# Performance work log

Measured on AMD Instinct MI355X. Metric: run time of the kernel, lower is better.

The kernel has to match this reference:

```python
import jax, jax.numpy as jnp
import numpy as np
from jax import lax

LN_EPS = 1e-5

def _conv1d(h, w, b):
    # h: [N, L, Cin], w: [Cout, Cin, K] (torch Conv1d layout), padding=1
    out = lax.conv_general_dilated(h, w, window_strides=(1,), padding=[(1, 1)],
                                   dimension_numbers=("NWC", "OIW", "NWC"))
    return out + b

def _layer_norm(h, g, b):
    m = jnp.mean(h, axis=-1, keepdims=True)
    v = jnp.mean((h - m) ** 2, axis=-1, keepdims=True)
    return (h - m) * lax.rsqrt(v + LN_EPS) * g + b

def setup_inputs() -> dict:
    key = jax.random.key(0)
    ks = jax.random.split(key, 8)
    N, L, D, F = 32, 512, 384, 256
    return {
        "x": jax.random.normal(ks[0], (N, L, D), jnp.float32),
        "conv1_w": jax.random.normal(ks[1], (F, D, 3), jnp.float32) * 0.05,
        "conv1_b": jnp.zeros((F,), jnp.float32),
        "ln1_g": jnp.ones((F,), jnp.float32),
        "ln1_b": jnp.zeros((F,), jnp.float32),
        "conv2_w": jax.random.normal(ks[2], (F, F, 3), jnp.float32) * 0.05,
        "conv2_b": jnp.zeros((F,), jnp.float32),
        "ln2_g": jnp.ones((F,), jnp.float32),
        "ln2_b": jnp.zeros((F,), jnp.float32),
        "lin_w": jax.random.normal(ks[3], (F,), jnp.float32) * 0.05,
        "lin_b": jnp.zeros((), jnp.float32),
        "target": jax.random.randint(ks[4], (N, L), 0, 8, dtype=jnp.int32),
        "mel_max_length": 2048,
    }

def reference(x, conv1_w, conv1_b, ln1_g, ln1_b, conv2_w, conv2_b, ln2_g, ln2_b,
              lin_w, lin_b, target, mel_max_length):
    # Duration predictor (dropout is identity at inference)
    h = jax.nn.relu(_layer_norm(_conv1d(x, conv1_w, conv1_b), ln1_g, ln1_b))
    h = jax.nn.relu(_layer_norm(_conv1d(h, conv2_w, conv2_b), ln2_g, ln2_b))
    duration_predictor_output = jnp.einsum("nlf,f->nl", h, lin_w) + lin_b  # [N, L]

    # LR: frame t copies phoneme j iff cumsum(dur)[:j] <= t < cumsum(dur)[:j+1]
    # (equivalent to the one-hot alignment matmul, padded to mel_max_length)
    N, L, D = x.shape
    T = mel_max_length
    cums = jnp.cumsum(target, axis=-1)                      # [N, L]
    frames = jnp.arange(T, dtype=cums.dtype)                # [T]
    idx = jax.vmap(lambda c: jnp.searchsorted(c, frames, side="right"))(cums)  # [N, T]
    valid = frames[None, :] < cums[:, -1:]                  # frames beyond total are zero
    gathered = jnp.take_along_axis(x, jnp.clip(idx, 0, L - 1)[:, :, None], axis=1)
    output = gathered * valid[:, :, None].astype(x.dtype)   # [N, T, D]
    return output, duration_predictor_output
```

## Files before the change

### kernel.cpp

```cpp
#include <hip/hip_runtime.h>
#include <hip/hip_bf16.h>

typedef unsigned short u16;
typedef short s8v __attribute__((ext_vector_type(8)));
typedef float f4v __attribute__((ext_vector_type(4)));
typedef u16 u16x8 __attribute__((ext_vector_type(8)));

static __device__ __forceinline__ u16 f2bf(float v) {
    __hip_bfloat16 h = __float2bfloat16(v);
    return *(u16*)&h;
}

__global__ __launch_bounds__(256) void gather_prep_kernel(
    const float* __restrict__ x,
    const int*   __restrict__ target,
    const float* __restrict__ w1,
    const float* __restrict__ w2,
    u16* __restrict__ Wt1,
    u16* __restrict__ Wt2,
    float* __restrict__ out0)
{
    __shared__ int c[512];
    __shared__ int ridx[64];
    const int b = blockIdx.x, tid = threadIdx.x;

    if (b >= 1024) {
        if (b < 2176) {
            const int K = 1152, DIN = 384;
            int e = (b - 1024) * 256 + tid;
            int f = e / K;
            int rem = e - f * K;
            int kc = rem / DIN;
            int d = rem - kc * DIN;
            Wt1[e] = f2bf(w1[f * K + d * 3 + kc]);
        } else {
            const int K = 768, DIN = 256;
            int e = (b - 2176) * 256 + tid;
            int f = e / K;
            int rem = e - f * K;
            int kc = rem / DIN;
            int d = rem - kc * DIN;
            Wt2[e] = f2bf(w2[f * K + d * 3 + kc]);
        }
        return;
    }

    const int n = b >> 5, sub = b & 31;
    c[tid]       = target[n * 512 + tid];
    c[tid + 256] = target[n * 512 + 256 + tid];
    __syncthreads();
    for (int off = 1; off < 512; off <<= 1) {
        int v0 = (tid       >= off) ? c[tid       - off] : 0;
        int v1 = (tid + 256 >= off) ? c[tid + 256 - off] : 0;
        __syncthreads();
        c[tid]       += v0;
        c[tid + 256] += v1;
        __syncthreads();
    }
    const int total = c[511];
    if (tid < 64) {
        int t = sub * 64 + tid;
        int lo = 0, hi = 512;
        while (lo < hi) {
            int mid = (lo + hi) >> 1;
            if (c[mid] <= t) lo = mid + 1; else hi = mid;
        }
        ridx[tid] = (t < total) ? min(lo, 511) : -1;
    }
    __syncthreads();

    const size_t xbase = (size_t)(n << 9) * 384;
    const size_t obase = ((size_t)(n << 11) + sub * 64) * 384;
    #pragma unroll 4
    for (int it = 0; it < 12; ++it) {
        int u  = tid + it * 256;
        int j  = u % 48;
        int rl = u / 48;
        int ie = ridx[rl];
        f4v v0 = {0.f, 0.f, 0.f, 0.f}, v1 = v0;
        if (ie >= 0) {
            const float* src = &x[xbase + (size_t)ie * 384];
            v0 = *(const f4v*)&src[j * 4];
            v1 = *(const f4v*)&src[(j + 48) * 4];
        }
        float* dst = &out0[obase + (size_t)rl * 384];
        __builtin_nontemporal_store(v0, (f4v*)&dst[j * 4]);
        __builtin_nontemporal_store(v1, (f4v*)&dst[(j + 48) * 4]);
    }
}

__global__ __launch_bounds__(256, 2) void fused_conv_kernel(
    const float* __restrict__ x,
    const u16* __restrict__ Wt1,
    const u16* __restrict__ Wt2,
    const float* __restrict__ cb1, const float* __restrict__ g1,
    const float* __restrict__ bb1,
    const float* __restrict__ cb2, const float* __restrict__ g2,
    const float* __restrict__ bb2,
    const float* __restrict__ lw, const float* __restrict__ lbp,
    float* __restrict__ dpo)
{
    __shared__ __align__(128) char LDS[73216];
    char* Bs    = LDS + 38400;
    float* redS = (float*)(LDS + 71168);
    float* redQ = (float*)(LDS + 71936);
    float* redP = (float*)(LDS + 72704);

    const int tid  = threadIdx.x;
    const int lane = tid & 63, wc = tid >> 6;
    const int lr = lane & 15, q4 = lane >> 4;
    const int sb = (blockIdx.x & 7) * 64 + (blockIdx.x >> 3);
    const int m0 = sb * 32;
    const int n  = m0 >> 9, l0 = m0 & 511;

    const int b_r    = tid >> 3;
    const int b_slot = (tid & 7) ^ (b_r & 7);
    int boff[4];
    #pragma unroll
    for (int ni = 0; ni < 4; ni++) boff[ni] = (64 * wc + 16 * ni + lr) * 128;
    const int slot0 = ((q4)     ^ (lr & 7)) << 4;
    const int slot1 = ((q4 | 4) ^ (lr & 7)) << 4;

    for (int u = tid; u < 2400; u += 256) {
        int j = u / 48, s = u - j * 48;
        int lp = l0 - 9 + j;
        f4v v0 = {0.f, 0.f, 0.f, 0.f}, v1 = v0;
        if (lp >= 0 && lp < 512) {
            const float* src = x + ((size_t)((n << 9) + lp)) * 384 + s * 8;
            v0 = *(const f4v*)src;
            v1 = *(const f4v*)(src + 4);
        }
        u16x8 r;
        #pragma unroll
        for (int jj = 0; jj < 4; jj++) { r[jj] = f2bf(v0[jj]); r[4 + jj] = f2bf(v1[jj]); }
        int ss = (s & ~7) | ((s & 7) ^ (j & 7));
        *(u16x8*)(LDS + j * 768 + ss * 16) = r;
    }

    auto xwread = [&](int j, int s) -> s8v {
        int ss = (s & ~7) | ((s & 7) ^ (j & 7));
        return *(const s8v*)(LDS + j * 768 + (ss << 4));
    };

    f4v acc[3][4];
    #pragma unroll
    for (int mi = 0; mi < 3; mi++)
        #pragma unroll
        for (int ni = 0; ni < 4; ni++) acc[mi][ni] = {0.f, 0.f, 0.f, 0.f};

    for (int t = 0; t < 18; ++t) {
        __syncthreads();
        const int k0 = t * 64;
        const u16* bsrc = Wt1 + (size_t)b_r * 1152 + k0 + b_slot * 8;
        #pragma unroll
        for (int q = 0; q < 8; q++) {
            __builtin_amdgcn_global_load_lds(
                (const __attribute__((address_space(1))) void*)(bsrc + (size_t)q * 32 * 1152),
                (__attribute__((address_space(3))) void*)(Bs + q * 4096 + tid * 16),
                16, 0, 0);
        }
        __syncthreads();

        const int kc = k0 / 384;
        const int s0 = (k0 - kc * 384) >> 3;
        #pragma unroll
        for (int kk = 0; kk < 2; kk++) {
            const int sl = kk ? slot1 : slot0;
            const int s  = s0 + 4 * kk + q4;
            s8v a0 = xwread(lr + kc,      s);
            s8v a1 = xwread(16 + lr + kc, s);
            s8v a2 = xwread(32 + lr + kc, s);
            s8v b0 = *(const s8v*)(Bs + boff[0] + sl);
            s8v b1 = *(const s8v*)(Bs + boff[1] + sl);
            s8v b2 = *(const s8v*)(Bs + boff[2] + sl);
            s8v b3 = *(const s8v*)(Bs + boff[3] + sl);
            acc[0][0] = __builtin_amdgcn_mfma_f32_16x16x32_bf16(a0, b0, acc[0][0], 0, 0, 0);
            acc[0][1] = __builtin_amdgcn_mfma_f32_16x16x32_bf16(a0, b1, acc[0][1], 0, 0, 0);
            acc[0][2] = __builtin_amdgcn_mfma_f32_16x16x32_bf16(a0, b2, acc[0][2], 0, 0, 0);
            acc[0][3] = __builtin_amdgcn_mfma_f32_16x16x32_bf16(a0, b3, acc[0][3], 0, 0, 0);
            acc[1][0] = __builtin_amdgcn_mfma_f32_16x16x32_bf16(a1, b0, acc[1][0], 0, 0, 0);
            acc[1][1] = __builtin_amdgcn_mfma_f32_16x16x32_bf16(a1, b1, acc[1][1], 0, 0, 0);
            acc[1][2] = __builtin_amdgcn_mfma_f32_16x16x32_bf16(a1, b2, acc[1][2], 0, 0, 0);
            acc[1][3] = __builtin_amdgcn_mfma_f32_16x16x32_bf16(a1, b3, acc[1][3], 0, 0, 0);
            acc[2][0] = __builtin_amdgcn_mfma_f32_16x16x32_bf16(a2, b0, acc[2][0], 0, 0, 0);
            acc[2][1] = __builtin_amdgcn_mfma_f32_16x16x32_bf16(a2, b1, acc[2][1], 0, 0, 0);
            acc[2][2] = __builtin_amdgcn_mfma_f32_16x16x32_bf16(a2, b2, acc[2][2], 0, 0, 0);
            acc[2][3] = __builtin_amdgcn_mfma_f32_16x16x32_bf16(a2, b3, acc[2][3], 0, 0, 0);
        }
    }

    int col[4];
    float cbv[4], gv[4], bbv[4];
    #pragma unroll
    for (int ni = 0; ni < 4; ni++) {
        col[ni] = 64 * wc + 16 * ni + lr;
        cbv[ni] = cb1[col[ni]]; gv[ni] = g1[col[ni]]; bbv[ni] = bb1[col[ni]];
    }

    #pragma unroll
    for (int mi = 0; mi < 3; mi++)
        #pragma unroll
        for (int reg = 0; reg < 4; reg++) {
            float s = 0.f, q = 0.f;
            #pragma unroll
            for (int ni = 0; ni < 4; ni++) {
                float v = acc[mi][ni][reg] + cbv[ni];
                s += v; q += v * v;
            }
            #pragma unroll
            for (int msk = 1; msk < 16; msk <<= 1) {
                s += __shfl_xor(s, msk);
                q += __shfl_xor(q, msk);
            }
            if (lr == 0) {
                int rl = 16 * mi + 4 * q4 + reg;
                redS[rl * 4 + wc] = s;
                redQ[rl * 4 + wc] = q;
            }
        }
    __syncthreads();

    #pragma unroll
    for (int mi = 0; mi < 3; mi++)
        #pragma unroll
        for (int reg = 0; reg < 4; reg++) {
            int rl = 16 * mi + 4 * q4 + reg;
            int h  = rl - 7;
            if (h >= 0 && h < 34) {
                float4 ps = *(float4*)&redS[rl * 4];
                float4 pq = *(float4*)&redQ[rl * 4];
                float mean = (ps.x + ps.y + ps.z + ps.w) * (1.f / 256.f);
                float var  = (pq.x + pq.y + pq.z + pq.w) * (1.f / 256.f) - mean * mean;
                float rs   = rsqrtf(var + 1e-5f);
                int l = l0 - 8 + rl;
                bool lv = (l >= 0 && l < 512);
                #pragma unroll
                for (int ni = 0; ni < 4; ni++) {
                    float v = acc[mi][ni][reg] + cbv[ni];
                    float o = lv ? fmaxf(0.f, (v - mean) * rs * gv[ni] + bbv[ni]) : 0.f;
                    int slot = (col[ni] >> 3) ^ (h & 7);
                    *(u16*)(LDS + h * 512 + slot * 16 + (col[ni] & 7) * 2) = f2bf(o);
                }
            }
        }

    f4v acc2[2][4];
    #pragma unroll
    for (int mi = 0; mi < 2; mi++)
        #pragma unroll
        for (int ni = 0; ni < 4; ni++) acc2[mi][ni] = {0.f, 0.f, 0.f, 0.f};

    for (int t2 = 0; t2 < 12; ++t2) {
        __syncthreads();
        const int k0 = t2 * 64;
        const u16* bsrc = Wt2 + (size_t)b_r * 768 + k0 + b_slot * 8;
        #pragma unroll
        for (int q = 0; q < 8; q++) {
            __builtin_amdgcn_global_load_lds(
                (const __attribute__((address_space(1))) void*)(bsrc + (size_t)q * 32 * 768),
                (__attribute__((address_space(3))) void*)(Bs + q * 4096 + tid * 16),
                16, 0, 0);
        }
        __syncthreads();

        const int kc2   = t2 >> 2;
        const int sbase = 8 * (t2 & 3);
        #pragma unroll
        for (int kk = 0; kk < 2; kk++) {
            const int sl = kk ? slot1 : slot0;
            s8v b0 = *(const s8v*)(Bs + boff[0] + sl);
            s8v b1 = *(const s8v*)(Bs + boff[1] + sl);
            s8v b2 = *(const s8v*)(Bs + boff[2] + sl);
            s8v b3 = *(const s8v*)(Bs + boff[3] + sl);
            s8v a0, a1;
            {
                int h = lr + kc2;
                int s = sbase + 4 * kk + q4;
                a0 = *(const s8v*)(LDS + h * 512 + ((s ^ (h & 7)) << 4));
                h = 16 + lr + kc2;
                a1 = *(const s8v*)(LDS + h * 512 + ((s ^ (h & 7)) << 4));
            }
            acc2[0][0] = __builtin_amdgcn_mfma_f32_16x16x32_bf16(a0, b0, acc2[0][0], 0, 0, 0);
            acc2[0][1] = __builtin_amdgcn_mfma_f32_16x16x32_bf16(a0, b1, acc2[0][1], 0, 0, 0);
            acc2[0][2] = __builtin_amdgcn_mfma_f32_16x16x32_bf16(a0, b2, acc2[0][2], 0, 0, 0);
            acc2[0][3] = __builtin_amdgcn_mfma_f32_16x16x32_bf16(a0, b3, acc2[0][3], 0, 0, 0);
            acc2[1][0] = __builtin_amdgcn_mfma_f32_16x16x32_bf16(a1, b0, acc2[1][0], 0, 0, 0);
            acc2[1][1] = __builtin_amdgcn_mfma_f32_16x16x32_bf16(a1, b1, acc2[1][1], 0, 0, 0);
            acc2[1][2] = __builtin_amdgcn_mfma_f32_16x16x32_bf16(a1, b2, acc2[1][2], 0, 0, 0);
            acc2[1][3] = __builtin_amdgcn_mfma_f32_16x16x32_bf16(a1, b3, acc2[1][3], 0, 0, 0);
        }
    }

    float cbv2[4], gv2[4], bbv2[4], lwv[4];
    #pragma unroll
    for (int ni = 0; ni < 4; ni++) {
        cbv2[ni] = cb2[col[ni]]; gv2[ni] = g2[col[ni]]; bbv2[ni] = bb2[col[ni]];
        lwv[ni]  = lw[col[ni]];
    }

    float sv[2][4], sq[2][4];
    #pragma unroll
    for (int mi = 0; mi < 2; mi++)
        #pragma unroll
        for (int reg = 0; reg < 4; reg++) {
            float s = 0.f, q = 0.f;
            #pragma unroll
            for (int ni = 0; ni < 4; ni++) {
                float v = acc2[mi][ni][reg] + cbv2[ni];
                s += v; q += v * v;
            }
            #pragma unroll
            for (int msk = 1; msk < 16; msk <<= 1) {
                s += __shfl_xor(s, msk);
                q += __shfl_xor(q, msk);
            }
            sv[mi][reg] = s; sq[mi][reg] = q;
        }
    __syncthreads();
    if (lr == 0) {
        #pragma unroll
        for (int mi = 0; mi < 2; mi++)
            #pragma unroll
            for (int reg = 0; reg < 4; reg++) {
                int rl = 16 * mi + 4 * q4 + reg;
                redS[rl * 4 + wc] = sv[mi][reg];
                redQ[rl * 4 + wc] = sq[mi][reg];
            }
    }
    __syncthreads();

    float pp[2][4];
    #pragma unroll
    for (int mi = 0; mi < 2; mi++)
        #pragma unroll
        for (int reg = 0; reg < 4; reg++) {
            int rl = 16 * mi + 4 * q4 + reg;
            float4 ps = *(float4*)&redS[rl * 4];
            float4 pq = *(float4*)&redQ[rl * 4];
            float mean = (ps.x + ps.y + ps.z + ps.w) * (1.f / 256.f);
            float var  = (pq.x + pq.y + pq.z + pq.w) * (1.f / 256.f) - mean * mean;
            float rs   = rsqrtf(var + 1e-5f);
            float p = 0.f;
            #pragma unroll
            for (int ni = 0; ni < 4; ni++) {
                float v = acc2[mi][ni][reg] + cbv2[ni];
                float o = fmaxf(0.f, (v - mean) * rs * gv2[ni] + bbv2[ni]);
                p += o * lwv[ni];
            }
            #pragma unroll
            for (int msk = 1; msk < 16; msk <<= 1) p += __shfl_xor(p, msk);
            pp[mi][reg] = p;
        }
    if (lr == 0) {
        #pragma unroll
        for (int mi = 0; mi < 2; mi++)
            #pragma unroll
            for (int reg = 0; reg < 4; reg++) {
                int rl = 16 * mi + 4 * q4 + reg;
                redP[rl * 4 + wc] = pp[mi][reg];
            }
    }
    __syncthreads();
    if (tid < 32) {
        float4 p4 = *(float4*)&redP[tid * 4];
        dpo[m0 + tid] = p4.x + p4.y + p4.z + p4.w + lbp[0];
    }
}

extern "C" void kernel_launch(void* const* d_in, const int* in_sizes, int n_in,
                              void* d_out, int out_size, void* d_ws, size_t ws_size,
                              hipStream_t stream) {
    const float* x   = (const float*)d_in[0];
    const float* w1  = (const float*)d_in[1];
    const float* b1  = (const float*)d_in[2];
    const float* g1  = (const float*)d_in[3];
    const float* bb1 = (const float*)d_in[4];
    const float* w2  = (const float*)d_in[5];
    const float* b2  = (const float*)d_in[6];
    const float* g2  = (const float*)d_in[7];
    const float* bb2 = (const float*)d_in[8];
    const float* lw  = (const float*)d_in[9];
    const float* lb  = (const float*)d_in[10];
    const int* target = (const int*)d_in[11];

    char* wsb = (char*)d_ws;
    u16*  Wt1 = (u16*)wsb;
    u16*  Wt2 = (u16*)(wsb + 589824);

    float* out0 = (float*)d_out;
    float* dpo  = out0 + (size_t)32 * 2048 * 384;

    gather_prep_kernel<<<2944, 256, 0, stream>>>(
        x, target, w1, w2, Wt1, Wt2, out0);

    fused_conv_kernel<<<512, 256, 0, stream>>>(
        x, Wt1, Wt2, b1, g1, bb1, b2, g2, bb2, lw, lb, dpo);
}
```

Measured before the change: 67.65 us.

## Double-buffer weight tiles with half-size K steps in both conv GEMM loops

Replaces the single 32KB weight tile (K=64 per step, two syncs per step) with two 16KB buffers holding K=32 each. The next tile's global-to-LDS load is issued before computing on the current one, so weight fetch latency overlaps the MFMA work and each step needs only one barrier. The LDS swizzle is changed to fit the 64-byte row layout. In exchange there are twice as many iterations and barriers per step, and each step has less MFMA work to hide the load behind. The code also appears to rely on the barrier at the end of each iteration to cover the async LDS load's completion, with no explicit wait on it.

```diff
diff --git a/kernel.cpp b/kernel.cpp
--- a/kernel.cpp
+++ b/kernel.cpp
@@ -101,7 +101,7 @@
     float* __restrict__ dpo)
 {
     __shared__ __align__(128) char LDS[73216];
-    char* Bs    = LDS + 38400;
+    char* Bs0   = LDS + 38400;
     float* redS = (float*)(LDS + 71168);
     float* redQ = (float*)(LDS + 71936);
     float* redP = (float*)(LDS + 72704);
@@ -113,13 +113,12 @@
     const int m0 = sb * 32;
     const int n  = m0 >> 9, l0 = m0 & 511;
 
-    const int b_r    = tid >> 3;
-    const int b_slot = (tid & 7) ^ (b_r & 7);
+    const int b_r32   = tid >> 2;
+    const int b_slot32 = (tid & 3) ^ ((tid >> 3) & 3);
     int boff[4];
     #pragma unroll
-    for (int ni = 0; ni < 4; ni++) boff[ni] = (64 * wc + 16 * ni + lr) * 128;
-    const int slot0 = ((q4)     ^ (lr & 7)) << 4;
-    const int slot1 = ((q4 | 4) ^ (lr & 7)) << 4;
+    for (int ni = 0; ni < 4; ni++) boff[ni] = (64 * wc + 16 * ni + lr) * 64;
+    const int bslot = (q4 ^ ((lr >> 1) & 3)) << 4;
 
     for (int u = tid; u < 2400; u += 256) {
         int j = u / 48, s = u - j * 48;
@@ -142,38 +141,41 @@
         return *(const s8v*)(LDS + j * 768 + (ss << 4));
     };
 
-    f4v acc[3][4];
-    #pragma unroll
-    for (int mi = 0; mi < 3; mi++)
-        #pragma unroll
-        for (int ni = 0; ni < 4; ni++) acc[mi][ni] = {0.f, 0.f, 0.f, 0.f};
-
-    for (int t = 0; t < 18; ++t) {
-        __syncthreads();
-        const int k0 = t * 64;
-        const u16* bsrc = Wt1 + (size_t)b_r * 1152 + k0 + b_slot * 8;
-        #pragma unroll
-        for (int q = 0; q < 8; q++) {
+    auto stageB = [&](const u16* __restrict__ Wt, int K, int buf, int t) {
+        const int k0 = t * 32;
+        const u16* bsrc = Wt + (size_t)b_r32 * K + k0 + b_slot32 * 8;
+        char* Bs = Bs0 + buf * 16384;
+        #pragma unroll
+        for (int q = 0; q < 4; q++) {
             __builtin_amdgcn_global_load_lds(
-                (const __attribute__((address_space(1))) void*)(bsrc + (size_t)q * 32 * 1152),
+                (const __attribute__((address_space(1))) void*)(bsrc + (size_t)q * 64 * K),
                 (__attribute__((address_space(3))) void*)(Bs + q * 4096 + tid * 16),
                 16, 0, 0);
         }
-        __syncthreads();
-
-        const int kc = k0 / 384;
-        const int s0 = (k0 - kc * 384) >> 3;
-        #pragma unroll
-        for (int kk = 0; kk < 2; kk++) {
-            const int sl = kk ? slot1 : slot0;
-            const int s  = s0 + 4 * kk + q4;
+    };
+
+    f4v acc[3][4];
+    #pragma unroll
+    for (int mi = 0; mi < 3; mi++)
+        #pragma unroll
+        for (int ni = 0; ni < 4; ni++) acc[mi][ni] = {0.f, 0.f, 0.f, 0.f};
+
+    stageB(Wt1, 1152, 0, 0);
+    __syncthreads();
+    int cur = 0;
+    for (int t = 0; t < 36; ++t) {
+        if (t + 1 < 36) stageB(Wt1, 1152, cur ^ 1, t + 1);
+        {
+            char* Bs = Bs0 + cur * 16384;
+            const int kc = t / 12;
+            const int s  = (t % 12) * 4 + q4;
             s8v a0 = xwread(lr + kc,      s);
             s8v a1 = xwread(16 + lr + kc, s);
             s8v a2 = xwread(32 + lr + kc, s);
-            s8v b0 = *(const s8v*)(Bs + boff[0] + sl);
-            s8v b1 = *(const s8v*)(Bs + boff[1] + sl);
-            s8v b2 = *(const s8v*)(Bs + boff[2] + sl);
-            s8v b3 = *(const s8v*)(Bs + boff[3] + sl);
+            s8v b0 = *(const s8v*)(Bs + boff[0] + bslot);
+            s8v b1 = *(const s8v*)(Bs + boff[1] + bslot);
+            s8v b2 = *(const s8v*)(Bs + boff[2] + bslot);
+            s8v b3 = *(const s8v*)(Bs + boff[3] + bslot);
             acc[0][0] = __builtin_amdgcn_mfma_f32_16x16x32_bf16(a0, b0, acc[0][0], 0, 0, 0);
             acc[0][1] = __builtin_amdgcn_mfma_f32_16x16x32_bf16(a0, b1, acc[0][1], 0, 0, 0);
             acc[0][2] = __builtin_amdgcn_mfma_f32_16x16x32_bf16(a0, b2, acc[0][2], 0, 0, 0);
@@ -187,6 +189,8 @@
             acc[2][2] = __builtin_amdgcn_mfma_f32_16x16x32_bf16(a2, b2, acc[2][2], 0, 0, 0);
             acc[2][3] = __builtin_amdgcn_mfma_f32_16x16x32_bf16(a2, b3, acc[2][3], 0, 0, 0);
         }
+        __syncthreads();
+        cur ^= 1;
     }
 
     int col[4];
@@ -250,32 +254,22 @@
         #pragma unroll
         for (int ni = 0; ni < 4; ni++) acc2[mi][ni] = {0.f, 0.f, 0.f, 0.f};
 
-    for (int t2 = 0; t2 < 12; ++t2) {
-        __syncthreads();
-        const int k0 = t2 * 64;
-        const u16* bsrc = Wt2 + (size_t)b_r * 768 + k0 + b_slot * 8;
-        #pragma unroll
-        for (int q = 0; q < 8; q++) {
-            __builtin_amdgcn_global_load_lds(
-                (const __attribute__((address_space(1))) void*)(bsrc + (size_t)q * 32 * 768),
-                (__attribute__((address_space(3))) void*)(Bs + q * 4096 + tid * 16),
-                16, 0, 0);
-        }
-        __syncthreads();
-
-        const int kc2   = t2 >> 2;
-        const int sbase = 8 * (t2 & 3);
-        #pragma unroll
-        for (int kk = 0; kk < 2; kk++) {
-            const int sl = kk ? slot1 : slot0;
-            s8v b0 = *(const s8v*)(Bs + boff[0] + sl);
-            s8v b1 = *(const s8v*)(Bs + boff[1] + sl);
-            s8v b2 = *(const s8v*)(Bs + boff[2] + sl);
-            s8v b3 = *(const s8v*)(Bs + boff[3] + sl);
+    stageB(Wt2, 768, 0, 0);
+    __syncthreads();
+    cur = 0;
+    for (int t2 = 0; t2 < 24; ++t2) {
+        if (t2 + 1 < 24) stageB(Wt2, 768, cur ^ 1, t2 + 1);
+        {
+            char* Bs = Bs0 + cur * 16384;
+            const int kc2 = t2 >> 3;
+            const int s   = (t2 & 7) * 4 + q4;
+            s8v b0 = *(const s8v*)(Bs + boff[0] + bslot);
+            s8v b1 = *(const s8v*)(Bs + boff[1] + bslot);
+            s8v b2 = *(const s8v*)(Bs + boff[2] + bslot);
+            s8v b3 = *(const s8v*)(Bs + boff[3] + bslot);
             s8v a0, a1;
             {
                 int h = lr + kc2;
-                int s = sbase + 4 * kk + q4;
                 a0 = *(const s8v*)(LDS + h * 512 + ((s ^ (h & 7)) << 4));
                 h = 16 + lr + kc2;
                 a1 = *(const s8v*)(LDS + h * 512 + ((s ^ (h & 7)) << 4));
@@ -289,6 +283,8 @@
             acc2[1][2] = __builtin_amdgcn_mfma_f32_16x16x32_bf16(a1, b2, acc2[1][2], 0, 0, 0);
             acc2[1][3] = __builtin_amdgcn_mfma_f32_16x16x32_bf16(a1, b3, acc2[1][3], 0, 0, 0);
         }
+        __syncthreads();
+        cur ^= 1;
     }
 
     float cbv2[4], gv2[4], bbv2[4], lwv[4];
```

Result: slower. 74.41 us (+10.0%).

## Register-prefetch weight tiles and shrink input halo staging in fused conv kernel

Applied to the files above, without the earlier changes.

Replaces the synchronous global_load_lds weight staging with register prefetch of the next K-tile. The loads are issued before the current tile's MFMAs and written to LDS afterwards, so global latency overlaps compute. The x staging buffer is cut from 50 to 36 rows by storing only the 34 rows with real data and clamping reads of the halo rows. Those halo rows only feed conv1 rows that are zeroed or never used. The smaller LDS footprint may allow higher occupancy, at the cost of extra VGPRs for the prefetch registers and a clamp on every A read.

```diff
diff --git a/kernel.cpp b/kernel.cpp
--- a/kernel.cpp
+++ b/kernel.cpp
@@ -100,11 +100,11 @@
     const float* __restrict__ lw, const float* __restrict__ lbp,
     float* __restrict__ dpo)
 {
-    __shared__ __align__(128) char LDS[73216];
-    char* Bs    = LDS + 38400;
-    float* redS = (float*)(LDS + 71168);
-    float* redQ = (float*)(LDS + 71936);
-    float* redP = (float*)(LDS + 72704);
+    __shared__ __align__(128) char LDS[62464];
+    char* Bs    = LDS + 27648;
+    float* redS = (float*)(LDS + 60416);
+    float* redQ = (float*)(LDS + 61184);
+    float* redP = (float*)(LDS + 61952);
 
     const int tid  = threadIdx.x;
     const int lane = tid & 63, wc = tid >> 6;
@@ -121,9 +121,22 @@
     const int slot0 = ((q4)     ^ (lr & 7)) << 4;
     const int slot1 = ((q4 | 4) ^ (lr & 7)) << 4;
 
-    for (int u = tid; u < 2400; u += 256) {
-        int j = u / 48, s = u - j * 48;
-        int lp = l0 - 9 + j;
+    auto loadB = [&](const u16* __restrict__ Wt, int K, int t, s8v* bv) {
+        const int k0 = t * 64;
+        const u16* bsrc = Wt + (size_t)b_r * K + k0 + b_slot * 8;
+        #pragma unroll
+        for (int q = 0; q < 8; q++)
+            bv[q] = *(const s8v*)(bsrc + (size_t)q * 32 * K);
+    };
+    auto writeB = [&](const s8v* bv) {
+        #pragma unroll
+        for (int q = 0; q < 8; q++)
+            *(s8v*)(Bs + q * 4096 + tid * 16) = bv[q];
+    };
+
+    for (int u = tid; u < 1728; u += 256) {
+        int j7 = u / 48, s = u - j7 * 48;
+        int lp = l0 - 2 + j7;
         f4v v0 = {0.f, 0.f, 0.f, 0.f}, v1 = v0;
         if (lp >= 0 && lp < 512) {
             const float* src = x + ((size_t)((n << 9) + lp)) * 384 + s * 8;
@@ -133,13 +146,14 @@
         u16x8 r;
         #pragma unroll
         for (int jj = 0; jj < 4; jj++) { r[jj] = f2bf(v0[jj]); r[4 + jj] = f2bf(v1[jj]); }
-        int ss = (s & ~7) | ((s & 7) ^ (j & 7));
-        *(u16x8*)(LDS + j * 768 + ss * 16) = r;
+        int ss = (s & ~7) | ((s & 7) ^ (j7 & 7));
+        *(u16x8*)(LDS + j7 * 768 + ss * 16) = r;
     }
 
     auto xwread = [&](int j, int s) -> s8v {
-        int ss = (s & ~7) | ((s & 7) ^ (j & 7));
-        return *(const s8v*)(LDS + j * 768 + (ss << 4));
+        int j7 = min(max(j, 7), 42) - 7;
+        int ss = (s & ~7) | ((s & 7) ^ (j7 & 7));
+        return *(const s8v*)(LDS + j7 * 768 + (ss << 4));
     };
 
     f4v acc[3][4];
@@ -148,44 +162,50 @@
         #pragma unroll
         for (int ni = 0; ni < 4; ni++) acc[mi][ni] = {0.f, 0.f, 0.f, 0.f};
 
+    {
+        s8v bv[8];
+        loadB(Wt1, 1152, 0, bv);
+        writeB(bv);
+    }
+    __syncthreads();
+
     for (int t = 0; t < 18; ++t) {
+        s8v nv[8];
+        const bool pre = (t + 1 < 18);
+        if (pre) loadB(Wt1, 1152, t + 1, nv);
+        {
+            const int k0 = t * 64;
+            const int kc = k0 / 384;
+            const int s0 = (k0 - kc * 384) >> 3;
+            #pragma unroll
+            for (int kk = 0; kk < 2; kk++) {
+                const int sl = kk ? slot1 : slot0;
+                const int s  = s0 + 4 * kk + q4;
+                s8v a0 = xwread(lr + kc,      s);
+                s8v a1 = xwread(16 + lr + kc, s);
+                s8v a2 = xwread(32 + lr + kc, s);
+                s8v b0 = *(const s8v*)(Bs + boff[0] + sl);
+                s8v b1 = *(const s8v*)(Bs + boff[1] + sl);
+                s8v b2 = *(const s8v*)(Bs + boff[2] + sl);
+                s8v b3 = *(const s8v*)(Bs + boff[3] + sl);
+                acc[0][0] = __builtin_amdgcn_mfma_f32_16x16x32_bf16(a0, b0, acc[0][0], 0, 0, 0);
+                acc[0][1] = __builtin_amdgcn_mfma_f32_16x16x32_bf16(a0, b1, acc[0][1], 0, 0, 0);
+                acc[0][2] = __builtin_amdgcn_mfma_f32_16x16x32_bf16(a0, b2, acc[0][2], 0, 0, 0);
+                acc[0][3] = __builtin_amdgcn_mfma_f32_16x16x32_bf16(a0, b3, acc[0][3], 0, 0, 0);
+                acc[1][0] = __builtin_amdgcn_mfma_f32_16x16x32_bf16(a1, b0, acc[1][0], 0, 0, 0);
+                acc[1][1] = __builtin_amdgcn_mfma_f32_16x16x32_bf16(a1, b1, acc[1][1], 0, 0, 0);
+                acc[1][2] = __builtin_amdgcn_mfma_f32_16x16x32_bf16(a1, b2, acc[1][2], 0, 0, 0);
+                acc[1][3] = __builtin_amdgcn_mfma_f32_16x16x32_bf16(a1, b3, acc[1][3], 0, 0, 0);
+                acc[2][0] = __builtin_amdgcn_mfma_f32_16x16x32_bf16(a2, b0, acc[2][0], 0, 0, 0);
+                acc[2][1] = __builtin_amdgcn_mfma_f32_16x16x32_bf16(a2, b1, acc[2][1], 0, 0, 0);
+                acc[2][2] = __builtin_amdgcn_mfma_f32_16x16x32_bf16(a2, b2, acc[2][2], 0, 0, 0);
+                acc[2][3] = __builtin_amdgcn_mfma_f32_16x16x32_bf16(a2, b3, acc[2][3], 0, 0, 0);
+            }
+        }
         __syncthreads();
-        const int k0 = t * 64;
-        const u16* bsrc = Wt1 + (size_t)b_r * 1152 + k0 + b_slot * 8;
-        #pragma unroll
-        for (int q = 0; q < 8; q++) {
-            __builtin_amdgcn_global_load_lds(
-                (const __attribute__((address_space(1))) void*)(bsrc + (size_t)q * 32 * 1152),
-                (__attribute__((address_space(3))) void*)(Bs + q * 4096 + tid * 16),
-                16, 0, 0);
-        }
-        __syncthreads();
-
-        const int kc = k0 / 384;
-        const int s0 = (k0 - kc * 384) >> 3;
-        #pragma unroll
-        for (int kk = 0; kk < 2; kk++) {
-            const int sl = kk ? slot1 : slot0;
-            const int s  = s0 + 4 * kk + q4;
-            s8v a0 = xwread(lr + kc,      s);
-            s8v a1 = xwread(16 + lr + kc, s);
-            s8v a2 = xwread(32 + lr + kc, s);
-            s8v b0 = *(const s8v*)(Bs + boff[0] + sl);
-            s8v b1 = *(const s8v*)(Bs + boff[1] + sl);
-            s8v b2 = *(const s8v*)(Bs + boff[2] + sl);
-            s8v b3 = *(const s8v*)(Bs + boff[3] + sl);
-            acc[0][0] = __builtin_amdgcn_mfma_f32_16x16x32_bf16(a0, b0, acc[0][0], 0, 0, 0);
-            acc[0][1] = __builtin_amdgcn_mfma_f32_16x16x32_bf16(a0, b1, acc[0][1], 0, 0, 0);
-            acc[0][2] = __builtin_amdgcn_mfma_f32_16x16x32_bf16(a0, b2, acc[0][2], 0, 0, 0);
-            acc[0][3] = __builtin_amdgcn_mfma_f32_16x16x32_bf16(a0, b3, acc[0][3], 0, 0, 0);
-            acc[1][0] = __builtin_amdgcn_mfma_f32_16x16x32_bf16(a1, b0, acc[1][0], 0, 0, 0);
-            acc[1][1] = __builtin_amdgcn_mfma_f32_16x16x32_bf16(a1, b1, acc[1][1], 0, 0, 0);
-            acc[1][2] = __builtin_amdgcn_mfma_f32_16x16x32_bf16(a1, b2, acc[1][2], 0, 0, 0);
-            acc[1][3] = __builtin_amdgcn_mfma_f32_16x16x32_bf16(a1, b3, acc[1][3], 0, 0, 0);
-            acc[2][0] = __builtin_amdgcn_mfma_f32_16x16x32_bf16(a2, b0, acc[2][0], 0, 0, 0);
-            acc[2][1] = __builtin_amdgcn_mfma_f32_16x16x32_bf16(a2, b1, acc[2][1], 0, 0, 0);
-            acc[2][2] = __builtin_amdgcn_mfma_f32_16x16x32_bf16(a2, b2, acc[2][2], 0, 0, 0);
-            acc[2][3] = __builtin_amdgcn_mfma_f32_16x16x32_bf16(a2, b3, acc[2][3], 0, 0, 0);
+        if (pre) {
+            writeB(nv);
+            __syncthreads();
         }
     }
 
@@ -250,44 +270,49 @@
         #pragma unroll
         for (int ni = 0; ni < 4; ni++) acc2[mi][ni] = {0.f, 0.f, 0.f, 0.f};
 
+    {
+        s8v bv[8];
+        loadB(Wt2, 768, 0, bv);
+        writeB(bv);
+    }
+    __syncthreads();
+
     for (int t2 = 0; t2 < 12; ++t2) {
+        s8v nv[8];
+        const bool pre = (t2 + 1 < 12);
+        if (pre) loadB(Wt2, 768, t2 + 1, nv);
+        {
+            const int kc2   = t2 >> 2;
+            const int sbase = 8 * (t2 & 3);
+            #pragma unroll
+            for (int kk = 0; kk < 2; kk++) {
+                const int sl = kk ? slot1 : slot0;
+                s8v b0 = *(const s8v*)(Bs + boff[0] + sl);
+                s8v b1 = *(const s8v*)(Bs + boff[1] + sl);
+                s8v b2 = *(const s8v*)(Bs + boff[2] + sl);
+                s8v b3 = *(const s8v*)(Bs + boff[3] + sl);
+                s8v a0, a1;
+                {
+                    int h = lr + kc2;
+                    int s = sbase + 4 * kk + q4;
+                    a0 = *(const s8v*)(LDS + h * 512 + ((s ^ (h & 7)) << 4));
+                    h = 16 + lr + kc2;
+                    a1 = *(const s8v*)(LDS + h * 512 + ((s ^ (h & 7)) << 4));
+                }
+                acc2[0][0] = __builtin_amdgcn_mfma_f32_16x16x32_bf16(a0, b0, acc2[0][0], 0, 0, 0);
+                acc2[0][1] = __builtin_amdgcn_mfma_f32_16x16x32_bf16(a0, b1, acc2[0][1], 0, 0, 0);
+                acc2[0][2] = __builtin_amdgcn_mfma_f32_16x16x32_bf16(a0, b2, acc2[0][2], 0, 0, 0);
+                acc2[0][3] = __builtin_amdgcn_mfma_f32_16x16x32_bf16(a0, b3, acc2[0][3], 0, 0, 0);
+                acc2[1][0] = __builtin_amdgcn_mfma_f32_16x16x32_bf16(a1, b0, acc2[1][0], 0, 0, 0);
+                acc2[1][1] = __builtin_amdgcn_mfma_f32_16x16x32_bf16(a1, b1, acc2[1][1], 0, 0, 0);
+                acc2[1][2] = __builtin_amdgcn_mfma_f32_16x16x32_bf16(a1, b2, acc2[1][2], 0, 0, 0);
+                acc2[1][3] = __builtin_amdgcn_mfma_f32_16x16x32_bf16(a1, b3, acc2[1][3], 0, 0, 0);
+            }
+        }
         __syncthreads();
-        const int k0 = t2 * 64;
-        const u16* bsrc = Wt2 + (size_t)b_r * 768 + k0 + b_slot * 8;
-        #pragma unroll
-        for (int q = 0; q < 8; q++) {
-            __builtin_amdgcn_global_load_lds(
-                (const __attribute__((address_space(1))) void*)(bsrc + (size_t)q * 32 * 768),
-                (__attribute__((address_space(3))) void*)(Bs + q * 4096 + tid * 16),
-                16, 0, 0);
-        }
-        __syncthreads();
-
-        const int kc2   = t2 >> 2;
-        const int sbase = 8 * (t2 & 3);
-        #pragma unroll
-        for (int kk = 0; kk < 2; kk++) {
-            const int sl = kk ? slot1 : slot0;
-            s8v b0 = *(const s8v*)(Bs + boff[0] + sl);
-            s8v b1 = *(const s8v*)(Bs + boff[1] + sl);
-            s8v b2 = *(const s8v*)(Bs + boff[2] + sl);
-            s8v b3 = *(const s8v*)(Bs + boff[3] + sl);
-            s8v a0, a1;
-            {
-                int h = lr + kc2;
-                int s = sbase + 4 * kk + q4;
-                a0 = *(const s8v*)(LDS + h * 512 + ((s ^ (h & 7)) << 4));
-                h = 16 + lr + kc2;
-                a1 = *(const s8v*)(LDS + h * 512 + ((s ^ (h & 7)) << 4));
-            }
-            acc2[0][0] = __builtin_amdgcn_mfma_f32_16x16x32_bf16(a0, b0, acc2[0][0], 0, 0, 0);
-            acc2[0][1] = __builtin_amdgcn_mfma_f32_16x16x32_bf16(a0, b1, acc2[0][1], 0, 0, 0);
-            acc2[0][2] = __builtin_amdgcn_mfma_f32_16x16x32_bf16(a0, b2, acc2[0][2], 0, 0, 0);
-            acc2[0][3] = __builtin_amdgcn_mfma_f32_16x16x32_bf16(a0, b3, acc2[0][3], 0, 0, 0);
-            acc2[1][0] = __builtin_amdgcn_mfma_f32_16x16x32_bf16(a1, b0, acc2[1][0], 0, 0, 0);
-            acc2[1][1] = __builtin_amdgcn_mfma_f32_16x16x32_bf16(a1, b1, acc2[1][1], 0, 0, 0);
-            acc2[1][2] = __builtin_amdgcn_mfma_f32_16x16x32_bf16(a1, b2, acc2[1][2], 0, 0, 0);
-            acc2[1][3] = __builtin_amdgcn_mfma_f32_16x16x32_bf16(a1, b3, acc2[1][3], 0, 0, 0);
+        if (pre) {
+            writeB(nv);
+            __syncthreads();
         }
     }
 
```

Result: no change. 67.52 us (-0.2%).

## Split fused conv kernel across 8 waves and shrink the staged x window

Applied to the files above, without the earlier changes.

Doubles the fused conv block from 4 to 8 waves, so each wave computes 32 output channels instead of 64. This halves per-wave accumulators and B-fragment loads and gives more waves to hide latency. The staged x window is trimmed to only the rows the computation actually reads (36 instead of 50), with index clamping in the reader, which cuts LDS use and global loads. LayerNorm partial reductions now sum over 8 waves, and the extra waves add synchronisation cost and share the same MFMA units.

```diff
diff --git a/kernel.cpp b/kernel.cpp
--- a/kernel.cpp
+++ b/kernel.cpp
@@ -89,7 +89,7 @@
     }
 }
 
-__global__ __launch_bounds__(256, 2) void fused_conv_kernel(
+__global__ __launch_bounds__(512, 2) void fused_conv_kernel(
     const float* __restrict__ x,
     const u16* __restrict__ Wt1,
     const u16* __restrict__ Wt2,
@@ -100,14 +100,14 @@
     const float* __restrict__ lw, const float* __restrict__ lbp,
     float* __restrict__ dpo)
 {
-    __shared__ __align__(128) char LDS[73216];
-    char* Bs    = LDS + 38400;
-    float* redS = (float*)(LDS + 71168);
-    float* redQ = (float*)(LDS + 71936);
-    float* redP = (float*)(LDS + 72704);
+    __shared__ __align__(128) char LDS[64512];
+    char* Bs    = LDS + 27648;
+    float* redS = (float*)(LDS + 60416);
+    float* redQ = (float*)(LDS + 61952);
+    float* redP = (float*)(LDS + 63488);
 
     const int tid  = threadIdx.x;
-    const int lane = tid & 63, wc = tid >> 6;
+    const int lane = tid & 63, w = tid >> 6;
     const int lr = lane & 15, q4 = lane >> 4;
     const int sb = (blockIdx.x & 7) * 64 + (blockIdx.x >> 3);
     const int m0 = sb * 32;
@@ -115,15 +115,15 @@
 
     const int b_r    = tid >> 3;
     const int b_slot = (tid & 7) ^ (b_r & 7);
-    int boff[4];
-    #pragma unroll
-    for (int ni = 0; ni < 4; ni++) boff[ni] = (64 * wc + 16 * ni + lr) * 128;
+    int boff[2];
+    #pragma unroll
+    for (int ni = 0; ni < 2; ni++) boff[ni] = (32 * w + 16 * ni + lr) * 128;
     const int slot0 = ((q4)     ^ (lr & 7)) << 4;
     const int slot1 = ((q4 | 4) ^ (lr & 7)) << 4;
 
-    for (int u = tid; u < 2400; u += 256) {
-        int j = u / 48, s = u - j * 48;
-        int lp = l0 - 9 + j;
+    for (int u = tid; u < 1728; u += 512) {
+        int j7 = u / 48, s = u - j7 * 48;
+        int lp = l0 - 2 + j7;
         f4v v0 = {0.f, 0.f, 0.f, 0.f}, v1 = v0;
         if (lp >= 0 && lp < 512) {
             const float* src = x + ((size_t)((n << 9) + lp)) * 384 + s * 8;
@@ -133,34 +133,39 @@
         u16x8 r;
         #pragma unroll
         for (int jj = 0; jj < 4; jj++) { r[jj] = f2bf(v0[jj]); r[4 + jj] = f2bf(v1[jj]); }
-        int ss = (s & ~7) | ((s & 7) ^ (j & 7));
-        *(u16x8*)(LDS + j * 768 + ss * 16) = r;
+        int ss = (s & ~7) | ((s & 7) ^ (j7 & 7));
+        *(u16x8*)(LDS + j7 * 768 + ss * 16) = r;
     }
 
     auto xwread = [&](int j, int s) -> s8v {
-        int ss = (s & ~7) | ((s & 7) ^ (j & 7));
-        return *(const s8v*)(LDS + j * 768 + (ss << 4));
+        int j7 = min(max(j, 7), 42) - 7;
+        int ss = (s & ~7) | ((s & 7) ^ (j7 & 7));
+        return *(const s8v*)(LDS + j7 * 768 + (ss << 4));
     };
 
-    f4v acc[3][4];
+    auto stageB = [&](const u16* __restrict__ Wt, int K, int t) {
+        const int k0 = t * 64;
+        const u16* bsrc = Wt + (size_t)b_r * K + k0 + b_slot * 8;
+        #pragma unroll
+        for (int q = 0; q < 4; q++) {
+            __builtin_amdgcn_global_load_lds(
+                (const __attribute__((address_space(1))) void*)(bsrc + (size_t)q * 64 * K),
+                (__attribute__((address_space(3))) void*)(Bs + q * 8192 + tid * 16),
+                16, 0, 0);
+        }
+    };
+
+    f4v acc[3][2];
     #pragma unroll
     for (int mi = 0; mi < 3; mi++)
         #pragma unroll
-        for (int ni = 0; ni < 4; ni++) acc[mi][ni] = {0.f, 0.f, 0.f, 0.f};
+        for (int ni = 0; ni < 2; ni++) acc[mi][ni] = {0.f, 0.f, 0.f, 0.f};
 
     for (int t = 0; t < 18; ++t) {
         __syncthreads();
+        stageB(Wt1, 1152, t);
+        __syncthreads();
         const int k0 = t * 64;
-        const u16* bsrc = Wt1 + (size_t)b_r * 1152 + k0 + b_slot * 8;
-        #pragma unroll
-        for (int q = 0; q < 8; q++) {
-            __builtin_amdgcn_global_load_lds(
-                (const __attribute__((address_space(1))) void*)(bsrc + (size_t)q * 32 * 1152),
-                (__attribute__((address_space(3))) void*)(Bs + q * 4096 + tid * 16),
-                16, 0, 0);
-        }
-        __syncthreads();
-
         const int kc = k0 / 384;
         const int s0 = (k0 - kc * 384) >> 3;
         #pragma unroll
@@ -172,28 +177,20 @@
             s8v a2 = xwread(32 + lr + kc, s);
             s8v b0 = *(const s8v*)(Bs + boff[0] + sl);
             s8v b1 = *(const s8v*)(Bs + boff[1] + sl);
-            s8v b2 = *(const s8v*)(Bs + boff[2] + sl);
-            s8v b3 = *(const s8v*)(Bs + boff[3] + sl);
             acc[0][0] = __builtin_amdgcn_mfma_f32_16x16x32_bf16(a0, b0, acc[0][0], 0, 0, 0);
             acc[0][1] = __builtin_amdgcn_mfma_f32_16x16x32_bf16(a0, b1, acc[0][1], 0, 0, 0);
-            acc[0][2] = __builtin_amdgcn_mfma_f32_16x16x32_bf16(a0, b2, acc[0][2], 0, 0, 0);
-            acc[0][3] = __builtin_amdgcn_mfma_f32_16x16x32_bf16(a0, b3, acc[0][3], 0, 0, 0);
             acc[1][0] = __builtin_amdgcn_mfma_f32_16x16x32_bf16(a1, b0, acc[1][0], 0, 0, 0);
             acc[1][1] = __builtin_amdgcn_mfma_f32_16x16x32_bf16(a1, b1, acc[1][1], 0, 0, 0);
-            acc[1][2] = __builtin_amdgcn_mfma_f32_16x16x32_bf16(a1, b2, acc[1][2], 0, 0, 0);
-            acc[1][3] = __builtin_amdgcn_mfma_f32_16x16x32_bf16(a1, b3, acc[1][3], 0, 0, 0);
             acc[2][0] = __builtin_amdgcn_mfma_f32_16x16x32_bf16(a2, b0, acc[2][0], 0, 0, 0);
             acc[2][1] = __builtin_amdgcn_mfma_f32_16x16x32_bf16(a2, b1, acc[2][1], 0, 0, 0);
-            acc[2][2] = __builtin_amdgcn_mfma_f32_16x16x32_bf16(a2, b2, acc[2][2], 0, 0, 0);
-            acc[2][3] = __builtin_amdgcn_mfma_f32_16x16x32_bf16(a2, b3, acc[2][3], 0, 0, 0);
-        }
-    }
-
-    int col[4];
-    float cbv[4], gv[4], bbv[4];
-    #pragma unroll
-    for (int ni = 0; ni < 4; ni++) {
-        col[ni] = 64 * wc + 16 * ni + lr;
+        }
+    }
+
+    int col[2];
+    float cbv[2], gv[2], bbv[2];
+    #pragma unroll
+    for (int ni = 0; ni < 2; ni++) {
+        col[ni] = 32 * w + 16 * ni + lr;
         cbv[ni] = cb1[col[ni]]; gv[ni] = g1[col[ni]]; bbv[ni] = bb1[col[ni]];
     }
 
@@ -203,7 +200,7 @@
         for (int reg = 0; reg < 4; reg++) {
             float s = 0.f, q = 0.f;
             #pragma unroll
-            for (int ni = 0; ni < 4; ni++) {
+            for (int ni = 0; ni < 2; ni++) {
                 float v = acc[mi][ni][reg] + cbv[ni];
                 s += v; q += v * v;
             }
@@ -214,8 +211,8 @@
             }
             if (lr == 0) {
                 int rl = 16 * mi + 4 * q4 + reg;
-                redS[rl * 4 + wc] = s;
-                redQ[rl * 4 + wc] = q;
+                redS[rl * 8 + w] = s;
+                redQ[rl * 8 + w] = q;
             }
         }
     __syncthreads();
@@ -227,15 +224,19 @@
             int rl = 16 * mi + 4 * q4 + reg;
             int h  = rl - 7;
             if (h >= 0 && h < 34) {
-                float4 ps = *(float4*)&redS[rl * 4];
-                float4 pq = *(float4*)&redQ[rl * 4];
-                float mean = (ps.x + ps.y + ps.z + ps.w) * (1.f / 256.f);
-                float var  = (pq.x + pq.y + pq.z + pq.w) * (1.f / 256.f) - mean * mean;
+                float4 p0 = *(float4*)&redS[rl * 8];
+                float4 p1 = *(float4*)&redS[rl * 8 + 4];
+                float4 q0 = *(float4*)&redQ[rl * 8];
+                float4 q1 = *(float4*)&redQ[rl * 8 + 4];
+                float mean = (p0.x + p0.y + p0.z + p0.w + p1.x + p1.y + p1.z + p1.w)
+                             * (1.f / 256.f);
+                float var  = (q0.x + q0.y + q0.z + q0.w + q1.x + q1.y + q1.z + q1.w)
+                             * (1.f / 256.f) - mean * mean;
                 float rs   = rsqrtf(var + 1e-5f);
                 int l = l0 - 8 + rl;
                 bool lv = (l >= 0 && l < 512);
                 #pragma unroll
-                for (int ni = 0; ni < 4; ni++) {
+                for (int ni = 0; ni < 2; ni++) {
                     float v = acc[mi][ni][reg] + cbv[ni];
                     float o = lv ? fmaxf(0.f, (v - mean) * rs * gv[ni] + bbv[ni]) : 0.f;
                     int slot = (col[ni] >> 3) ^ (h & 7);
@@ -244,25 +245,16 @@
             }
         }
 
-    f4v acc2[2][4];
+    f4v acc2[2][2];
     #pragma unroll
     for (int mi = 0; mi < 2; mi++)
         #pragma unroll
-        for (int ni = 0; ni < 4; ni++) acc2[mi][ni] = {0.f, 0.f, 0.f, 0.f};
+        for (int ni = 0; ni < 2; ni++) acc2[mi][ni] = {0.f, 0.f, 0.f, 0.f};
 
     for (int t2 = 0; t2 < 12; ++t2) {
         __syncthreads();
-        const int k0 = t2 * 64;
-        const u16* bsrc = Wt2 + (size_t)b_r * 768 + k0 + b_slot * 8;
-        #pragma unroll
-        for (int q = 0; q < 8; q++) {
-            __builtin_amdgcn_global_load_lds(
-                (const __attribute__((address_space(1))) void*)(bsrc + (size_t)q * 32 * 768),
-                (__attribute__((address_space(3))) void*)(Bs + q * 4096 + tid * 16),
-                16, 0, 0);
-        }
-        __syncthreads();
-
+        stageB(Wt2, 768, t2);
+        __syncthreads();
         const int kc2   = t2 >> 2;
         const int sbase = 8 * (t2 & 3);
         #pragma unroll
@@ -270,8 +262,6 @@
             const int sl = kk ? slot1 : slot0;
             s8v b0 = *(const s8v*)(Bs + boff[0] + sl);
             s8v b1 = *(const s8v*)(Bs + boff[1] + sl);
-            s8v b2 = *(const s8v*)(Bs + boff[2] + sl);
-            s8v b3 = *(const s8v*)(Bs + boff[3] + sl);
             s8v a0, a1;
             {
                 int h = lr + kc2;
@@ -282,18 +272,14 @@
             }
             acc2[0][0] = __builtin_amdgcn_mfma_f32_16x16x32_bf16(a0, b0, acc2[0][0], 0, 0, 0);
             acc2[0][1] = __builtin_amdgcn_mfma_f32_16x16x32_bf16(a0, b1, acc2[0][1], 0, 0, 0);
-            acc2[0][2] = __builtin_amdgcn_mfma_f32_16x16x32_bf16(a0, b2, acc2[0][2], 0, 0, 0);
-            acc2[0][3] = __builtin_amdgcn_mfma_f32_16x16x32_bf16(a0, b3, acc2[0][3], 0, 0, 0);
             acc2[1][0] = __builtin_amdgcn_mfma_f32_16x16x32_bf16(a1, b0, acc2[1][0], 0, 0, 0);
             acc2[1][1] = __builtin_amdgcn_mfma_f32_16x16x32_bf16(a1, b1, acc2[1][1], 0, 0, 0);
-            acc2[1][2] = __builtin_amdgcn_mfma_f32_16x16x32_bf16(a1, b2, acc2[1][2], 0, 0, 0);
-            acc2[1][3] = __builtin_amdgcn_mfma_f32_16x16x32_bf16(a1, b3, acc2[1][3], 0, 0, 0);
-        }
-    }
-
-    float cbv2[4], gv2[4], bbv2[4], lwv[4];
-    #pragma unroll
-    for (int ni = 0; ni < 4; ni++) {
+        }
+    }
+
+    float cbv2[2], gv2[2], bbv2[2], lwv[2];
+    #pragma unroll
+    for (int ni = 0; ni < 2; ni++) {
         cbv2[ni] = cb2[col[ni]]; gv2[ni] = g2[col[ni]]; bbv2[ni] = bb2[col[ni]];
         lwv[ni]  = lw[col[ni]];
     }
@@ -305,7 +291,7 @@
         for (int reg = 0; reg < 4; reg++) {
             float s = 0.f, q = 0.f;
             #pragma unroll
-            for (int ni = 0; ni < 4; ni++) {
+            for (int ni = 0; ni < 2; ni++) {
                 float v = acc2[mi][ni][reg] + cbv2[ni];
                 s += v; q += v * v;
             }
@@ -323,8 +309,8 @@
             #pragma unroll
             for (int reg = 0; reg < 4; reg++) {
                 int rl = 16 * mi + 4 * q4 + reg;
-                redS[rl * 4 + wc] = sv[mi][reg];
-                redQ[rl * 4 + wc] = sq[mi][reg];
+                redS[rl * 8 + w] = sv[mi][reg];
+                redQ[rl * 8 + w] = sq[mi][reg];
             }
     }
     __syncthreads();
@@ -335,14 +321,18 @@
         #pragma unroll
         for (int reg = 0; reg < 4; reg++) {
             int rl = 16 * mi + 4 * q4 + reg;
-            float4 ps = *(float4*)&redS[rl * 4];
-            float4 pq = *(float4*)&redQ[rl * 4];
-            float mean = (ps.x + ps.y + ps.z + ps.w) * (1.f / 256.f);
-            float var  = (pq.x + pq.y + pq.z + pq.w) * (1.f / 256.f) - mean * mean;
+            float4 p0 = *(float4*)&redS[rl * 8];
+            float4 p1 = *(float4*)&redS[rl * 8 + 4];
+            float4 q0 = *(float4*)&redQ[rl * 8];
+            float4 q1 = *(float4*)&redQ[rl * 8 + 4];
+            float mean = (p0.x + p0.y + p0.z + p0.w + p1.x + p1.y + p1.z + p1.w)
+                         * (1.f / 256.f);
+            float var  = (q0.x + q0.y + q0.z + q0.w + q1.x + q1.y + q1.z + q1.w)
+                         * (1.f / 256.f) - mean * mean;
             float rs   = rsqrtf(var + 1e-5f);
             float p = 0.f;
             #pragma unroll
-            for (int ni = 0; ni < 4; ni++) {
+            for (int ni = 0; ni < 2; ni++) {
                 float v = acc2[mi][ni][reg] + cbv2[ni];
                 float o = fmaxf(0.f, (v - mean) * rs * gv2[ni] + bbv2[ni]);
                 p += o * lwv[ni];
@@ -357,13 +347,14 @@
             #pragma unroll
             for (int reg = 0; reg < 4; reg++) {
                 int rl = 16 * mi + 4 * q4 + reg;
-                redP[rl * 4 + wc] = pp[mi][reg];
+                redP[rl * 8 + w] = pp[mi][reg];
             }
     }
     __syncthreads();
     if (tid < 32) {
-        float4 p4 = *(float4*)&redP[tid * 4];
-        dpo[m0 + tid] = p4.x + p4.y + p4.z + p4.w + lbp[0];
+        float4 p0 = *(float4*)&redP[tid * 8];
+        float4 p1 = *(float4*)&redP[tid * 8 + 4];
+        dpo[m0 + tid] = p0.x + p0.y + p0.z + p0.w + p1.x + p1.y + p1.z + p1.w + lbp[0];
     }
 }
 
@@ -393,6 +384,6 @@
     gather_prep_kernel<<<2944, 256, 0, stream>>>(
         x, target, w1, w2, Wt1, Wt2, out0);
 
-    fused_conv_kernel<<<512, 256, 0, stream>>>(
+    fused_conv_kernel<<<512, 512, 0, stream>>>(
         x, Wt1, Wt2, b1, g1, bb1, b2, g2, bb2, lw, lb, dpo);
 }
```

Result: slower. 72.75 us (+7.5%).
